# Optimization experiments

Measured on AMD Instinct MI355X. Metric: run time of the kernel, lower is better.

The kernel has to match this reference:

```python
import jax, jax.numpy as jnp
import numpy as np

B, S, H = 2, 2048, 896
NH, NKV, D = 7, 1, 128
I = 4864
EPS = 1e-6


def rms_norm(x, w):
    var = jnp.mean(x * x, axis=-1, keepdims=True)
    return x * jax.lax.rsqrt(var + EPS) * w


def apply_rope(q, k, cos, sin):
    # q: [B,NH,S,D], k: [B,NKV,S,D]; cos/sin: [S,D]
    c = cos[None, None, :, : D // 2]
    s = sin[None, None, :, : D // 2]

    def rot(x):
        x1, x2 = x[..., : D // 2], x[..., D // 2 :]
        return jnp.concatenate([x1 * c - x2 * s, x1 * s + x2 * c], axis=-1)

    return rot(q), rot(k)


def setup_inputs() -> dict:
    key = jax.random.key(0)
    ks = jax.random.split(key, 12)
    sc = 0.02
    inp = {
        "hidden_states": jax.random.normal(ks[0], (B, S, H), jnp.float32),
        "wq": jax.random.normal(ks[1], (NH * D, H), jnp.float32) * sc,
        "bq": jnp.zeros((NH * D,), jnp.float32),
        "wk": jax.random.normal(ks[2], (NKV * D, H), jnp.float32) * sc,
        "bk": jnp.zeros((NKV * D,), jnp.float32),
        "wv": jax.random.normal(ks[3], (NKV * D, H), jnp.float32) * sc,
        "bv": jnp.zeros((NKV * D,), jnp.float32),
        "wo": jax.random.normal(ks[4], (H, NH * D), jnp.float32) * sc,
        "w_gate": jax.random.normal(ks[5], (I, H), jnp.float32) * sc,
        "w_up": jax.random.normal(ks[6], (I, H), jnp.float32) * sc,
        "w_down": jax.random.normal(ks[7], (H, I), jnp.float32) * sc,
        "ln1_w": jnp.ones((H,), jnp.float32),
        "ln2_w": jnp.ones((H,), jnp.float32),
    }
    # causal additive mask [1,1,S,S]
    neg = jnp.finfo(jnp.float32).min
    causal = jnp.tril(jnp.ones((S, S), bool))
    inp["attention_mask"] = jnp.where(causal, 0.0, neg)[None, None]
    # RoPE tables (base 10000), last dim = head_dim
    inv_freq = 1.0 / (10000.0 ** (np.arange(0, D, 2, dtype=np.float32) / D))
    freqs = np.arange(S, dtype=np.float32)[:, None] * inv_freq[None, :]
    emb = np.concatenate([freqs, freqs], axis=-1)  # [S,D]
    inp["cos"] = jnp.asarray(np.cos(emb))
    inp["sin"] = jnp.asarray(np.sin(emb))
    return inp


def reference(hidden_states, attention_mask, cos, sin, wq, bq, wk, bk, wv, bv,
              wo, w_gate, w_up, w_down, ln1_w, ln2_w):
    x = hidden_states
    residual = x
    h = rms_norm(x, ln1_w)
    # projections
    q = (h @ wq.T + bq).reshape(B, S, NH, D).transpose(0, 2, 1, 3)
    k = (h @ wk.T + bk).reshape(B, S, NKV, D).transpose(0, 2, 1, 3)
    v = (h @ wv.T + bv).reshape(B, S, NKV, D).transpose(0, 2, 1, 3)
    q, k = apply_rope(q, k, cos, sin)
    # GQA broadcast
    k = jnp.repeat(k, NH // NKV, axis=1)
    v = jnp.repeat(v, NH // NKV, axis=1)
    scale = D ** -0.5
    scores = jnp.einsum("bhqd,bhkd->bhqk", q, k) * scale + attention_mask
    attn = jax.nn.softmax(scores, axis=-1)
    out = jnp.einsum("bhqk,bhkd->bhqd", attn, v)
    out = out.transpose(0, 2, 1, 3).reshape(B, S, NH * D)
    attn_out = out @ wo.T
    x = residual + attn_out
    residual = x
    h = rms_norm(x, ln2_w)
    mlp = (jax.nn.silu(h @ w_gate.T) * (h @ w_up.T)) @ w_down.T
    return residual + mlp
```

## Files before the change

kernel.cpp:

```cpp
#include <hip/hip_runtime.h>
#include <stdint.h>
#include <stddef.h>


typedef unsigned short u16;
typedef unsigned long long u64;
typedef __bf16 bf16x8 __attribute__((ext_vector_type(8)));
typedef u16    u16x8  __attribute__((ext_vector_type(8)));
typedef float  f32x4  __attribute__((ext_vector_type(4)));

__device__ inline float b2f(u16 u) {
  union { unsigned int i; float f; } v; v.i = ((unsigned int)u) << 16; return v.f;
}
__device__ inline u16 f2b(float f) {
  union { float f; unsigned int i; } v; v.f = f;
  unsigned int r = v.i + 0x7FFFu + ((v.i >> 16) & 1u);
  return (u16)(r >> 16);
}

__device__ inline f32x4 mfma16(bf16x8 a, bf16x8 b, f32x4 c) {
  return __builtin_amdgcn_mfma_f32_16x16x32_bf16(a, b, c, 0, 0, 0);
}

__device__ inline void gload_lds16(const u16* g, u16* l) {
  __builtin_amdgcn_global_load_lds((__attribute__((address_space(1))) void*)g,
                                   (__attribute__((address_space(3))) void*)l,
                                   16, 0, 0);
}

template<int ITERS>
__device__ inline void stage_lds64(const u16* __restrict__ g, int ld, u16* lds, int t) {
  int wub = t & 192;
  #pragma unroll
  for (int i = 0; i < ITERS; ++i) {
    int e8 = i * 256 + t;
    int r = e8 >> 3, c = (e8 & 7) << 3;
    gload_lds16(g + (size_t)r * ld + c, lds + (i * 256 + wub) * 8);
  }
}

__global__ __launch_bounds__(256) void detect_k(const unsigned int* __restrict__ x,
                                                int* __restrict__ flag) {
  __shared__ int red[4];
  int t = threadIdx.x;
  int weird = 0;
  #pragma unroll
  for (int i = 0; i < 4; ++i) {
    unsigned int w = x[t * 4 + i];
    float a = fabsf(b2f((u16)(w & 0xFFFF)));
    if (!(a <= 1e5f)) weird++;
    else if (a != 0.0f && a < 1e-30f) weird++;
  }
  #pragma unroll
  for (int off = 32; off; off >>= 1) weird += __shfl_xor(weird, off);
  if ((t & 63) == 0) red[t >> 6] = weird;
  __syncthreads();
  if (t == 0) flag[0] = (red[0] + red[1] + red[2] + red[3] > 64) ? 1 : 0;
}

struct CvtJob { const void* src; u16* dst; int n; };
struct CvtJobs { CvtJob j[15]; };

__global__ __launch_bounds__(256) void convert_k(CvtJobs jobs, const int* __restrict__ flag) {
  CvtJob c = jobs.j[blockIdx.y];
  int idx = (blockIdx.x * 256 + threadIdx.x) * 8;
  if (idx >= c.n) return;
  if (*flag) {
    const float* s = (const float*)c.src;
    u16x8 o;
    #pragma unroll
    for (int i = 0; i < 8; ++i) o[i] = f2b(s[idx + i]);
    *(u16x8*)(c.dst + idx) = o;
  } else {
    *(u16x8*)(c.dst + idx) = *(const u16x8*)((const u16*)c.src + idx);
  }
}

__global__ __launch_bounds__(448) void rmsnorm_k(const u16* __restrict__ x,
                                                 const u16* __restrict__ w,
                                                 u16* __restrict__ out) {
  __shared__ float red[7];
  int t = threadIdx.x;
  size_t row = blockIdx.x;
  const u16* xr = x + row * 896;
  unsigned int pair = *(const unsigned int*)&xr[t * 2];
  float v0 = b2f((u16)(pair & 0xFFFF)), v1 = b2f((u16)(pair >> 16));
  float ss = v0 * v0 + v1 * v1;
  #pragma unroll
  for (int off = 32; off; off >>= 1) ss += __shfl_xor(ss, off);
  if ((t & 63) == 0) red[t >> 6] = ss;
  __syncthreads();
  float tot = red[0] + red[1] + red[2] + red[3] + red[4] + red[5] + red[6];
  float inv = rsqrtf(tot * (1.0f / 896.0f) + 1e-6f);
  unsigned int wp = *(const unsigned int*)&w[t * 2];
  unsigned int o = (unsigned int)f2b(v0 * inv * b2f((u16)(wp & 0xFFFF)))
                 | ((unsigned int)f2b(v1 * inv * b2f((u16)(wp >> 16))) << 16);
  *(unsigned int*)&out[row * 896 + t * 2] = o;
}

__global__ __launch_bounds__(256) void gemm_qkv(const u16* __restrict__ A,
    const u16* __restrict__ wq, const u16* __restrict__ bq,
    const u16* __restrict__ wk, const u16* __restrict__ bk,
    const u16* __restrict__ wv, const u16* __restrict__ bv,
    u16* __restrict__ C) {
  __shared__ u16 As[128 * 64], Bs[128 * 64];
  int t = threadIdx.x, lane = t & 63, w = t >> 6;
  int wm = w >> 1, wn = w & 1, lrow = lane & 15, lg = lane >> 4;
  int bx = blockIdx.x, row0 = blockIdx.y * 128;
  const u16 *W, *bias; int ocol;
  if (bx < 7)       { W = wq + (size_t)bx * 128 * 896; bias = bq + bx * 128; ocol = bx * 128; }
  else if (bx == 7) { W = wk; bias = bk; ocol = 896; }
  else              { W = wv; bias = bv; ocol = 1024; }

  f32x4 acc[4][4] = {};
  for (int kt = 0; kt < 896; kt += 64) {
    stage_lds64<4>(A + (size_t)row0 * 896 + kt, 896, As, t);
    stage_lds64<4>(W + kt, 896, Bs, t);
    __syncthreads();
    #pragma unroll
    for (int kk = 0; kk < 2; ++kk) {
      bf16x8 af[4], bf[4];
      #pragma unroll
      for (int m = 0; m < 4; ++m)
        af[m] = *(const bf16x8*)&As[(wm * 64 + m * 16 + lrow) * 64 + kk * 32 + lg * 8];
      #pragma unroll
      for (int n = 0; n < 4; ++n)
        bf[n] = *(const bf16x8*)&Bs[(wn * 64 + n * 16 + lrow) * 64 + kk * 32 + lg * 8];
      #pragma unroll
      for (int m = 0; m < 4; ++m)
        #pragma unroll
        for (int n = 0; n < 4; ++n)
          acc[m][n] = mfma16(af[m], bf[n], acc[m][n]);
    }
    __syncthreads();
  }
  #pragma unroll
  for (int m = 0; m < 4; ++m)
    #pragma unroll
    for (int n = 0; n < 4; ++n) {
      int col = wn * 64 + n * 16 + lrow;
      float bb = b2f(bias[col]);
      #pragma unroll
      for (int j = 0; j < 4; ++j) {
        size_t row = row0 + wm * 64 + m * 16 + lg * 4 + j;
        C[row * 1152 + ocol + col] = f2b(acc[m][n][j] + bb);
      }
    }
}

template<bool RES, bool DYNOUT>
__global__ __launch_bounds__(256) void gemm_bt(const u16* __restrict__ A,
    const u16* __restrict__ W, const u16* __restrict__ resid,
    void* __restrict__ Cp, const int* __restrict__ flag, int K, int ldc) {
  __shared__ u16 As[128 * 64], Bs[128 * 64];
  int t = threadIdx.x, lane = t & 63, w = t >> 6;
  int wm = w >> 1, wn = w & 1, lrow = lane & 15, lg = lane >> 4;
  int col0 = blockIdx.x * 128, row0 = blockIdx.y * 128;
  int f32out = DYNOUT ? *flag : 0;

  f32x4 acc[4][4] = {};
  for (int kt = 0; kt < K; kt += 64) {
    stage_lds64<4>(A + (size_t)row0 * K + kt, K, As, t);
    stage_lds64<4>(W + (size_t)col0 * K + kt, K, Bs, t);
    __syncthreads();
    #pragma unroll
    for (int kk = 0; kk < 2; ++kk) {
      bf16x8 af[4], bf[4];
      #pragma unroll
      for (int m = 0; m < 4; ++m)
        af[m] = *(const bf16x8*)&As[(wm * 64 + m * 16 + lrow) * 64 + kk * 32 + lg * 8];
      #pragma unroll
      for (int n = 0; n < 4; ++n)
        bf[n] = *(const bf16x8*)&Bs[(wn * 64 + n * 16 + lrow) * 64 + kk * 32 + lg * 8];
      #pragma unroll
      for (int m = 0; m < 4; ++m)
        #pragma unroll
        for (int n = 0; n < 4; ++n)
          acc[m][n] = mfma16(af[m], bf[n], acc[m][n]);
    }
    __syncthreads();
  }
  #pragma unroll
  for (int m = 0; m < 4; ++m)
    #pragma unroll
    for (int n = 0; n < 4; ++n) {
      int col = col0 + wn * 64 + n * 16 + lrow;
      #pragma unroll
      for (int j = 0; j < 4; ++j) {
        size_t row = row0 + wm * 64 + m * 16 + lg * 4 + j;
        float v = acc[m][n][j];
        if (RES) v += b2f(resid[row * (size_t)ldc + col]);
        if (DYNOUT && f32out) ((float*)Cp)[row * (size_t)ldc + col] = v;
        else                  ((u16*)Cp)[row * (size_t)ldc + col] = f2b(v);
      }
    }
}

__global__ __launch_bounds__(512, 2) void gemm_gateup256(const u16* __restrict__ A,
    const u16* __restrict__ Wg, const u16* __restrict__ Wu,
    u16* __restrict__ act) {
  __shared__ u16 Abuf[3][256 * 32];
  __shared__ u16 Bbuf[3][256 * 32];
  int t = threadIdx.x, lane = t & 63, w = t >> 6;
  int wm = w >> 2, wn = w & 3;
  int lrow = lane & 15, lg = lane >> 4;
  const int nbx = 38;
  int bid = blockIdx.x;
  int sw = (bid & 7) * 76 + (bid >> 3);
  int bx = sw % nbx, by = sw / nbx;
  int col0 = bx * 128, row0 = by * 256;
  const u16* Ab  = A  + (size_t)row0 * 896;
  const u16* Wgb = Wg + (size_t)col0 * 896;
  const u16* Wub = Wu + (size_t)col0 * 896;
  const int NT = 28;

  int sl = t;
  int sr = ((sl >> 3) << 1) | ((sl >> 2) & 1);
  int sk = (sl & 3) << 3;
  auto stage = [&](int tt, int buf) {
    const u16* ga = Ab + tt * 32;
    gload_lds16(ga + (size_t)sr * 896 + sk,          &Abuf[buf][(t & 448) * 8]);
    gload_lds16(ga + (size_t)(128 + sr) * 896 + sk,  &Abuf[buf][(512 + (t & 448)) * 8]);
    gload_lds16(Wgb + (size_t)sr * 896 + tt * 32 + sk, &Bbuf[buf][(t & 448) * 8]);
    gload_lds16(Wub + (size_t)sr * 896 + tt * 32 + sk, &Bbuf[buf][(512 + (t & 448)) * 8]);
  };

  f32x4 accg[8][2] = {}, accu[8][2] = {};
  stage(0, 0);
  stage(1, 1);
  int buf = 0;
  for (int tt = 0; tt < NT; ++tt) {
    if (tt == NT - 1) asm volatile("s_waitcnt vmcnt(0)" ::: "memory");
    else              asm volatile("s_waitcnt vmcnt(4)" ::: "memory");
    asm volatile("s_waitcnt lgkmcnt(0)" ::: "memory");
    __builtin_amdgcn_sched_barrier(0);
    __builtin_amdgcn_s_barrier();
    __builtin_amdgcn_sched_barrier(0);
    if (tt + 2 < NT) {
      int nb = buf + 2; if (nb >= 3) nb -= 3;
      stage(tt + 2, nb);
    }
    const u16* Ac = Abuf[buf];
    const u16* Bc = Bbuf[buf];
    bf16x8 af[8], bg[2], bu[2];
    #pragma unroll
    for (int m = 0; m < 8; ++m) {
      int r = wm * 128 + m * 16 + lrow;
      af[m] = *(const bf16x8*)&Ac[(((r >> 1) << 3) | ((r & 1) << 2) | lg) << 3];
    }
    #pragma unroll
    for (int n = 0; n < 2; ++n) {
      int r = wn * 32 + n * 16 + lrow;
      int l = ((r >> 1) << 3) | ((r & 1) << 2) | lg;
      bg[n] = *(const bf16x8*)&Bc[l << 3];
      bu[n] = *(const bf16x8*)&Bc[(512 + l) << 3];
    }
    __builtin_amdgcn_s_setprio(1);
    #pragma unroll
    for (int m = 0; m < 8; ++m)
      #pragma unroll
      for (int n = 0; n < 2; ++n) {
        accg[m][n] = mfma16(af[m], bg[n], accg[m][n]);
        accu[m][n] = mfma16(af[m], bu[n], accu[m][n]);
      }
    __builtin_amdgcn_s_setprio(0);
    ++buf; if (buf >= 3) buf -= 3;
  }
  #pragma unroll
  for (int m = 0; m < 8; ++m)
    #pragma unroll
    for (int n = 0; n < 2; ++n) {
      int col = col0 + wn * 32 + n * 16 + lrow;
      #pragma unroll
      for (int j = 0; j < 4; ++j) {
        size_t row = row0 + wm * 128 + m * 16 + lg * 4 + j;
        float g = accg[m][n][j], u = accu[m][n][j];
        act[row * 4864 + col] = f2b(g / (1.0f + __expf(-g)) * u);
      }
    }
}

__global__ __launch_bounds__(256) void rope_k(u16* __restrict__ qkv,
                                              const u16* __restrict__ cosb,
                                              const u16* __restrict__ sinb) {
  int t = threadIdx.x;
  int d = t & 63, hsub = t >> 6;
  int hidx = blockIdx.x * 4 + hsub;
  size_t row = blockIdx.y;
  int s = (int)(row & 2047);
  int cb = hidx < 7 ? hidx * 128 : 896;
  u16* p = qkv + row * 1152 + cb;
  float x1 = b2f(p[d]), x2 = b2f(p[d + 64]);
  float c = b2f(cosb[s * 128 + d]), sn = b2f(sinb[s * 128 + d]);
  p[d]      = f2b(x1 * c - x2 * sn);
  p[d + 64] = f2b(x1 * sn + x2 * c);
}

__device__ inline void stageK_sw(u16* dst, const u16* kb, int k0, int t) {
  #pragma unroll
  for (int i = 0; i < 4; ++i) {
    int c = i * 256 + t;
    int row = c >> 4;
    int colb = ((c & 15) << 4) ^ ((row & 7) << 4);
    gload_lds16(kb + (size_t)(k0 + row) * 1152 + (colb >> 1),
                dst + (i * 256 + (t & 192)) * 8);
  }
}
__device__ inline void loadV(u16x8* vr, const u16* vb, int k0, int t) {
  int kq = (t & 15) * 4, d0 = (t >> 4) * 8;
  #pragma unroll
  for (int i = 0; i < 4; ++i)
    vr[i] = *(const u16x8*)(vb + (size_t)(k0 + kq + i) * 1152 + d0);
}
__device__ inline void writeVt(u16* VtB, const u16x8* vr, int t) {
  int kq = (t & 15) * 4, d0 = (t >> 4) * 8;
  #pragma unroll
  for (int dj = 0; dj < 8; ++dj) {
    int d = d0 + dj;
    u64 val = (u64)vr[0][dj] | ((u64)vr[1][dj] << 16)
            | ((u64)vr[2][dj] << 32) | ((u64)vr[3][dj] << 48);
    *(u64*)((char*)VtB + ((d * 128 + kq * 2) ^ ((d & 7) << 4))) = val;
  }
}
__device__ inline bf16x8 ldSw(const u16* buf, int row, int stride, int colbyte) {
  int byte = (row * stride + colbyte) ^ ((row & 7) << 4);
  return *(const bf16x8*)((const char*)buf + byte);
}

__device__ inline void smax_tile(f32x4* sa, int q0, int k0, bool diag,
                                 float* m_run, float* l_run, f32x4* oa,
                                 u16* PsW, int lrow, int lg) {
  const float SC = 0.12753102f;
  float s[4][4], mx[4];
  #pragma unroll
  for (int j = 0; j < 4; ++j) {
    int qrow = q0 + lg * 4 + j;
    #pragma unroll
    for (int nf = 0; nf < 4; ++nf) {
      float v = sa[nf][j] * SC;
      if (diag && (k0 + nf * 16 + lrow > qrow)) v = -1e30f;
      s[nf][j] = v;
    }
    mx[j] = fmaxf(fmaxf(s[0][j], s[1][j]), fmaxf(s[2][j], s[3][j]));
  }
  #pragma unroll
  for (int off = 1; off < 16; off <<= 1)
    #pragma unroll
    for (int j = 0; j < 4; ++j) mx[j] = fmaxf(mx[j], __shfl_xor(mx[j], off));
  float ps[4];
  #pragma unroll
  for (int j = 0; j < 4; ++j) {
    float mn = fmaxf(m_run[j], mx[j]);
    float al = exp2f(m_run[j] - mn);
    m_run[j] = mn;
    float sum = 0.0f;
    #pragma unroll
    for (int nf = 0; nf < 4; ++nf) {
      float pv = exp2f(s[nf][j] - mn);
      s[nf][j] = pv; sum += pv;
    }
    ps[j] = sum;
    l_run[j] *= al;
    #pragma unroll
    for (int nf2 = 0; nf2 < 8; ++nf2) oa[nf2][j] *= al;
  }
  #pragma unroll
  for (int off = 1; off < 16; off <<= 1)
    #pragma unroll
    for (int j = 0; j < 4; ++j) ps[j] += __shfl_xor(ps[j], off);
  #pragma unroll
  for (int j = 0; j < 4; ++j) l_run[j] += ps[j];
  #pragma unroll
  for (int j = 0; j < 4; ++j) {
    int row = lg * 4 + j;
    #pragma unroll
    for (int nf = 0; nf < 4; ++nf) {
      int byte = (row * 128 + (nf * 16 + lrow) * 2) ^ ((row & 7) << 4);
      *(u16*)((char*)PsW + byte) = f2b(s[nf][j]);
    }
  }
}

__global__ __launch_bounds__(256) void attn_k(const u16* __restrict__ qkv,
                                              u16* __restrict__ out) {
  __shared__ u16 Ks[2][64 * 128];
  __shared__ u16 Vt[2][128 * 64];
  __shared__ u16 Ps[4][2][16 * 64];
  int t = threadIdx.x, lane = t & 63, w = t >> 6;
  int lrow = lane & 15, lg = lane >> 4;
  int p = blockIdx.x, bh = blockIdx.y;
  int b = bh / 7, h = bh % 7;
  int tA = p, tB = 31 - p;
  int qA = tA * 64 + w * 16, qB = tB * 64 + w * 16;
  const u16* base = qkv + (size_t)b * 2048 * 1152;
  const u16* kb = base + 896;
  const u16* vb = base + 1024;

  bf16x8 qfA[4], qfB[4];
  #pragma unroll
  for (int kk = 0; kk < 4; ++kk) {
    qfA[kk] = *(const bf16x8*)(base + (size_t)(qA + lrow) * 1152 + h * 128 + kk * 32 + lg * 8);
    qfB[kk] = *(const bf16x8*)(base + (size_t)(qB + lrow) * 1152 + h * 128 + kk * 32 + lg * 8);
  }
  f32x4 oaA[8] = {}, oaB[8] = {};
  float mA[4], lA[4], mB[4], lB[4];
  #pragma unroll
  for (int j = 0; j < 4; ++j) { mA[j] = -1e30f; lA[j] = 0.0f; mB[j] = -1e30f; lB[j] = 0.0f; }

  stageK_sw(Ks[0], kb, 0, t);
  { u16x8 vr[4]; loadV(vr, vb, 0, t); writeVt(Vt[0], vr, t); }
  __syncthreads();

  int cur = 0;
  int ktmax = tB;
  for (int kt = 0; kt <= ktmax; ++kt) {
    bool pre = kt < ktmax;
    u16x8 vr2[4];
    if (pre) { stageK_sw(Ks[cur ^ 1], kb, (kt + 1) * 64, t); loadV(vr2, vb, (kt + 1) * 64, t); }

    bool doA = (kt <= tA);
    int k0 = kt * 64;
    const u16* KsC = Ks[cur];
    const u16* VtC = Vt[cur];

    f32x4 saA[4] = {}, saB[4] = {};
    #pragma unroll
    for (int nf = 0; nf < 4; ++nf) {
      bf16x8 kf[4];
      #pragma unroll
      for (int kk = 0; kk < 4; ++kk)
        kf[kk] = ldSw(KsC, nf * 16 + lrow, 256, kk * 64 + lg * 16);
      #pragma unroll
      for (int kk = 0; kk < 4; ++kk)
        saB[nf] = mfma16(qfB[kk], kf[kk], saB[nf]);
      if (doA)
        #pragma unroll
        for (int kk = 0; kk < 4; ++kk)
          saA[nf] = mfma16(qfA[kk], kf[kk], saA[nf]);
    }

    if (doA) smax_tile(saA, qA, k0, kt == tA, mA, lA, oaA, Ps[w][0], lrow, lg);
    smax_tile(saB, qB, k0, kt == tB, mB, lB, oaB, Ps[w][1], lrow, lg);

    bf16x8 pfA[2], pfB[2];
    #pragma unroll
    for (int ks = 0; ks < 2; ++ks) {
      pfB[ks] = ldSw(Ps[w][1], lrow, 128, ks * 64 + lg * 16);
      if (doA) pfA[ks] = ldSw(Ps[w][0], lrow, 128, ks * 64 + lg * 16);
    }
    #pragma unroll
    for (int ks = 0; ks < 2; ++ks) {
      bf16x8 vf[8];
      #pragma unroll
      for (int nf2 = 0; nf2 < 8; ++nf2)
        vf[nf2] = ldSw(VtC, nf2 * 16 + lrow, 128, ks * 64 + lg * 16);
      #pragma unroll
      for (int nf2 = 0; nf2 < 8; ++nf2)
        oaB[nf2] = mfma16(pfB[ks], vf[nf2], oaB[nf2]);
      if (doA)
        #pragma unroll
        for (int nf2 = 0; nf2 < 8; ++nf2)
          oaA[nf2] = mfma16(pfA[ks], vf[nf2], oaA[nf2]);
    }

    if (pre) writeVt(Vt[cur ^ 1], vr2, t);
    __syncthreads();
    cur ^= 1;
  }

  #pragma unroll
  for (int tile = 0; tile < 2; ++tile) {
    int q0 = tile ? qB : qA;
    const f32x4* oa = tile ? oaB : oaA;
    const float* l = tile ? lB : lA;
    u16* ob = out + ((size_t)b * 2048 + q0) * 896 + h * 128;
    #pragma unroll
    for (int j = 0; j < 4; ++j) {
      float rl = 1.0f / l[j];
      #pragma unroll
      for (int nf2 = 0; nf2 < 8; ++nf2)
        ob[(size_t)(lg * 4 + j) * 896 + nf2 * 16 + lrow] = f2b(oa[nf2][j] * rl);
    }
  }
}

extern "C" void kernel_launch(void* const* d_in, const int* in_sizes, int n_in,
                              void* d_out, int out_size, void* d_ws, size_t ws_size,
                              hipStream_t stream) {
  const int nX = 4096 * 896, nWQ = 896 * 896, nBQ = 896, nWK = 128 * 896, nBK = 128;
  const int nWV = 128 * 896, nBV = 128, nWO = 896 * 896;
  const int nWG = 4864 * 896, nWU = 4864 * 896, nWD = 896 * 4864;
  const int nLN = 896, nCS = 2048 * 128;

  u16* ws = (u16*)d_ws;
  int* flag = (int*)ws;
  size_t off = 16;
  auto alloc = [&](size_t n) { u16* p = ws + off; off += n; return p; };
  u16* cx   = alloc(nX);
  u16* cwq  = alloc(nWQ);  u16* cbq = alloc(nBQ);
  u16* cwk  = alloc(nWK);  u16* cbk = alloc(nBK);
  u16* cwv  = alloc(nWV);  u16* cbv = alloc(nBV);
  u16* cwo  = alloc(nWO);
  u16* cwg  = alloc(nWG);  u16* cwu = alloc(nWU);  u16* cwd = alloc(nWD);
  u16* cln1 = alloc(nLN);  u16* cln2 = alloc(nLN);
  u16* ccos = alloc(nCS);  u16* csin = alloc(nCS);
  u16* h    = alloc(4096 * 896);
  u16* qkv  = alloc(4096 * 1152);
  u16* attn = alloc(4096 * 896);
  u16* x2   = alloc(4096 * 896);
  u16* act  = alloc((size_t)4096 * 4864);

  detect_k<<<1, 256, 0, stream>>>((const unsigned int*)d_in[0], flag);

  CvtJobs jobs;
  const void* srcs[15] = { d_in[0], d_in[1], d_in[2], d_in[3], d_in[4], d_in[5],
                           d_in[6], d_in[7], d_in[8], d_in[9], d_in[10],
                           d_in[11], d_in[12], d_in[14], d_in[15] };
  u16* dsts[15] = { cx, cwq, cbq, cwk, cbk, cwv, cbv, cwo, cwg, cwu, cwd,
                    cln1, cln2, ccos, csin };
  int  ns[15]   = { nX, nWQ, nBQ, nWK, nBK, nWV, nBV, nWO, nWG, nWU, nWD,
                    nLN, nLN, nCS, nCS };
  for (int i = 0; i < 15; ++i) { jobs.j[i].src = srcs[i]; jobs.j[i].dst = dsts[i]; jobs.j[i].n = ns[i]; }
  convert_k<<<dim3(2128, 15), 256, 0, stream>>>(jobs, flag);

  rmsnorm_k <<<4096, 448, 0, stream>>>(cx, cln1, h);
  gemm_qkv  <<<dim3(9, 32),  256, 0, stream>>>(h, cwq, cbq, cwk, cbk, cwv, cbv, qkv);
  rope_k    <<<dim3(2, 4096), 256, 0, stream>>>(qkv, ccos, csin);
  attn_k    <<<dim3(16, 14), 256, 0, stream>>>(qkv, attn);
  gemm_bt<true, false> <<<dim3(7, 32), 256, 0, stream>>>(attn, cwo, cx, (void*)x2, flag, 896, 896);
  rmsnorm_k <<<4096, 448, 0, stream>>>(x2, cln2, h);
  gemm_gateup256 <<<608, 512, 0, stream>>>(h, cwg, cwu, act);
  gemm_bt<true, true> <<<dim3(7, 32), 256, 0, stream>>>(act, cwd, x2, d_out, flag, 4864, 896);
}
```

Baseline: 592.5 us.

## Split-K the down projection and deepen gate/up LDS pipeline to four stages

The down-projection GEMM (K=4864) now runs as a two-way split-K launch of 448 blocks instead of 224. One half writes fp32 partials plus the residual, the other writes bf16 partials, and a new reduce kernel sums them into the output. The aim is better CU occupancy on the long-K GEMM. Separately, the gate/up GEMM moves from triple to quadruple LDS buffering with prefetch distance three, to hide global load latency. In exchange it costs one extra kernel launch, extra partial-result traffic, bf16 rounding of one partial, more LDS that may limit residency, and it reuses the h and attn scratch buffers.

```diff
diff --git a/kernel.cpp b/kernel.cpp
--- a/kernel.cpp
+++ b/kernel.cpp
@@ -7,6 +7,7 @@
 typedef unsigned long long u64;
 typedef __bf16 bf16x8 __attribute__((ext_vector_type(8)));
 typedef u16    u16x8  __attribute__((ext_vector_type(8)));
+typedef u16    u16x4  __attribute__((ext_vector_type(4)));
 typedef float  f32x4  __attribute__((ext_vector_type(4)));
 
 __device__ inline float b2f(u16 u) {
@@ -196,11 +197,73 @@
     }
 }
 
+__global__ __launch_bounds__(256) void gemm_down_splitk(const u16* __restrict__ A,
+    const u16* __restrict__ W, const u16* __restrict__ resid,
+    float* __restrict__ P0, u16* __restrict__ P1) {
+  __shared__ u16 As[128 * 64], Bs[128 * 64];
+  int t = threadIdx.x, lane = t & 63, w = t >> 6;
+  int wm = w >> 1, wn = w & 1, lrow = lane & 15, lg = lane >> 4;
+  int col0 = blockIdx.x * 128, row0 = blockIdx.y * 128;
+  int k0 = blockIdx.z * 2432;
+
+  f32x4 acc[4][4] = {};
+  for (int kt = 0; kt < 2432; kt += 64) {
+    stage_lds64<4>(A + (size_t)row0 * 4864 + k0 + kt, 4864, As, t);
+    stage_lds64<4>(W + (size_t)col0 * 4864 + k0 + kt, 4864, Bs, t);
+    __syncthreads();
+    #pragma unroll
+    for (int kk = 0; kk < 2; ++kk) {
+      bf16x8 af[4], bf[4];
+      #pragma unroll
+      for (int m = 0; m < 4; ++m)
+        af[m] = *(const bf16x8*)&As[(wm * 64 + m * 16 + lrow) * 64 + kk * 32 + lg * 8];
+      #pragma unroll
+      for (int n = 0; n < 4; ++n)
+        bf[n] = *(const bf16x8*)&Bs[(wn * 64 + n * 16 + lrow) * 64 + kk * 32 + lg * 8];
+      #pragma unroll
+      for (int m = 0; m < 4; ++m)
+        #pragma unroll
+        for (int n = 0; n < 4; ++n)
+          acc[m][n] = mfma16(af[m], bf[n], acc[m][n]);
+    }
+    __syncthreads();
+  }
+  #pragma unroll
+  for (int m = 0; m < 4; ++m)
+    #pragma unroll
+    for (int n = 0; n < 4; ++n) {
+      int col = col0 + wn * 64 + n * 16 + lrow;
+      #pragma unroll
+      for (int j = 0; j < 4; ++j) {
+        size_t row = row0 + wm * 64 + m * 16 + lg * 4 + j;
+        float v = acc[m][n][j];
+        if (blockIdx.z == 0) P0[row * 896 + col] = v + b2f(resid[row * 896 + col]);
+        else                 P1[row * 896 + col] = f2b(v);
+      }
+    }
+}
+
+__global__ __launch_bounds__(256) void reduce_out_k(const float* __restrict__ p0,
+    const u16* __restrict__ p1, void* __restrict__ outp, const int* __restrict__ flag) {
+  int i = (blockIdx.x * 256 + threadIdx.x) * 4;
+  float4 a = *(const float4*)(p0 + i);
+  u16x4 b = *(const u16x4*)(p1 + i);
+  float o0 = a.x + b2f(b[0]), o1 = a.y + b2f(b[1]);
+  float o2 = a.z + b2f(b[2]), o3 = a.w + b2f(b[3]);
+  if (*flag) {
+    float4 o = make_float4(o0, o1, o2, o3);
+    *(float4*)((float*)outp + i) = o;
+  } else {
+    u16x4 o = { f2b(o0), f2b(o1), f2b(o2), f2b(o3) };
+    *(u16x4*)((u16*)outp + i) = o;
+  }
+}
+
 __global__ __launch_bounds__(512, 2) void gemm_gateup256(const u16* __restrict__ A,
     const u16* __restrict__ Wg, const u16* __restrict__ Wu,
     u16* __restrict__ act) {
-  __shared__ u16 Abuf[3][256 * 32];
-  __shared__ u16 Bbuf[3][256 * 32];
+  __shared__ u16 Abuf[4][256 * 32];
+  __shared__ u16 Bbuf[4][256 * 32];
   int t = threadIdx.x, lane = t & 63, w = t >> 6;
   int wm = w >> 2, wn = w & 3;
   int lrow = lane & 15, lg = lane >> 4;
@@ -228,20 +291,19 @@
   f32x4 accg[8][2] = {}, accu[8][2] = {};
   stage(0, 0);
   stage(1, 1);
-  int buf = 0;
+  stage(2, 2);
   for (int tt = 0; tt < NT; ++tt) {
-    if (tt == NT - 1) asm volatile("s_waitcnt vmcnt(0)" ::: "memory");
-    else              asm volatile("s_waitcnt vmcnt(4)" ::: "memory");
+    int rem = NT - 1 - tt;
+    if (rem >= 2)      asm volatile("s_waitcnt vmcnt(8)" ::: "memory");
+    else if (rem == 1) asm volatile("s_waitcnt vmcnt(4)" ::: "memory");
+    else               asm volatile("s_waitcnt vmcnt(0)" ::: "memory");
     asm volatile("s_waitcnt lgkmcnt(0)" ::: "memory");
     __builtin_amdgcn_sched_barrier(0);
     __builtin_amdgcn_s_barrier();
     __builtin_amdgcn_sched_barrier(0);
-    if (tt + 2 < NT) {
-      int nb = buf + 2; if (nb >= 3) nb -= 3;
-      stage(tt + 2, nb);
-    }
-    const u16* Ac = Abuf[buf];
-    const u16* Bc = Bbuf[buf];
+    if (tt + 3 < NT) stage(tt + 3, (tt + 3) & 3);
+    const u16* Ac = Abuf[tt & 3];
+    const u16* Bc = Bbuf[tt & 3];
     bf16x8 af[8], bg[2], bu[2];
     #pragma unroll
     for (int m = 0; m < 8; ++m) {
@@ -264,7 +326,6 @@
         accu[m][n] = mfma16(af[m], bu[n], accu[m][n]);
       }
     __builtin_amdgcn_s_setprio(0);
-    ++buf; if (buf >= 3) buf -= 3;
   }
   #pragma unroll
   for (int m = 0; m < 8; ++m)
@@ -530,5 +591,6 @@
   gemm_bt<true, false> <<<dim3(7, 32), 256, 0, stream>>>(attn, cwo, cx, (void*)x2, flag, 896, 896);
   rmsnorm_k <<<4096, 448, 0, stream>>>(x2, cln2, h);
   gemm_gateup256 <<<608, 512, 0, stream>>>(h, cwg, cwu, act);
-  gemm_bt<true, true> <<<dim3(7, 32), 256, 0, stream>>>(act, cwd, x2, d_out, flag, 4864, 896);
-}
+  gemm_down_splitk <<<dim3(7, 32, 2), 256, 0, stream>>>(act, cwd, x2, (float*)h, attn);
+  reduce_out_k <<<3584, 256, 0, stream>>>((const float*)h, attn, d_out, flag);
+}
```

Result: faster. 546.1 us (-7.8%).
